# Kernel tuning notes

Hardware: AMD Instinct MI355X
Metric: run time of the kernel (lower is better)

Reference implementation:

```python
import jax, jax.numpy as jnp
import numpy as np

V, E, H = 50000, 300, 128
B, L, QL, NS = 64, 1024, 32, 16
ITERATIONS = 3


def _gru_cell(x, h, w_ih, w_hh, b_ih, b_hh):
    # PyTorch GRUCell math.
    gi = x @ w_ih.T + b_ih
    gh = h @ w_hh.T + b_hh
    i_r, i_z, i_n = jnp.split(gi, 3, axis=-1)
    h_r, h_z, h_n = jnp.split(gh, 3, axis=-1)
    r = jax.nn.sigmoid(i_r + h_r)
    z = jax.nn.sigmoid(i_z + h_z)
    n = jnp.tanh(i_n + r * h_n)
    return (1.0 - z) * n + z * h


def _gru_scan(x, w_ih, w_hh, b_ih, b_hh):
    # x: [B, T, E] -> all hidden states [B, T, H] (nn.GRU, batch_first, h0=0).
    gi = jnp.einsum('bte,ge->btg', x, w_ih) + b_ih  # precompute input gates
    hdim = w_hh.shape[1]

    def step(h, gi_t):
        gh = h @ w_hh.T + b_hh
        i_r, i_z, i_n = jnp.split(gi_t, 3, axis=-1)
        h_r, h_z, h_n = jnp.split(gh, 3, axis=-1)
        r = jax.nn.sigmoid(i_r + h_r)
        z = jax.nn.sigmoid(i_z + h_z)
        n = jnp.tanh(i_n + r * h_n)
        h = (1.0 - z) * n + z * h
        return h, h

    h0 = jnp.zeros((x.shape[0], hdim), x.dtype)
    _, hs = jax.lax.scan(step, h0, jnp.swapaxes(gi, 0, 1))
    return jnp.swapaxes(hs, 0, 1)


def setup_inputs() -> dict:
    key = jax.random.key(0)
    ks = jax.random.split(key, 16)
    x_stories = jax.random.randint(ks[0], (B, L), 1, V)
    # Exactly NS sentence-end marks per story (evenly spaced) -> equal sent counts.
    pos = jnp.arange(1, NS + 1) * (L // NS) - 1
    x_story_masks = jnp.zeros((B, L), bool).at[:, pos].set(True)
    x_questions = jax.random.randint(ks[1], (B, QL), 1, V)
    emb = jax.random.normal(ks[2], (V, E), jnp.float32) * 0.1
    s = float(1.0 / np.sqrt(H))
    u = lambda k, sh: jax.random.uniform(k, sh, jnp.float32, -s, s)
    return {
        'x_stories': x_stories,
        'x_story_masks': x_story_masks,
        'x_questions': x_questions,
        'n_sents': NS,
        'emb': emb,
        'enc_w_ih': u(ks[3], (3 * H, E)),
        'enc_w_hh': u(ks[4], (3 * H, H)),
        'enc_b_ih': u(ks[5], (3 * H,)),
        'enc_b_hh': u(ks[6], (3 * H,)),
        'gate_w': u(ks[7], (1, 4 * H)),
        'gate_b': u(ks[8], (1,)),
        'ep_w_ih': u(ks[9], (3 * H, H)),
        'ep_w_hh': u(ks[10], (3 * H, H)),
        'ep_b_ih': u(ks[11], (3 * H,)),
        'ep_b_hh': u(ks[12], (3 * H,)),
    }


def reference(x_stories, x_story_masks, x_questions, n_sents, emb,
              enc_w_ih, enc_w_hh, enc_b_ih, enc_b_hh,
              gate_w, gate_b, ep_w_ih, ep_w_hh, ep_b_ih, ep_b_hh):
    Bb, Ll = x_stories.shape
    enc_stories = _gru_scan(emb[x_stories], enc_w_ih, enc_w_hh, enc_b_ih, enc_b_hh)  # [B,L,H]
    # Gather the n_sents masked (sentence-end) hidden states per story, in order.
    ar = jnp.arange(Ll)
    sort_key = jnp.where(x_story_masks, ar, Ll + ar)
    idx = jnp.argsort(sort_key, axis=1)[:, :n_sents]  # [B,NS]
    sents = jnp.take_along_axis(enc_stories, idx[:, :, None], axis=1)  # [B,NS,H]
    # Question encoding; pick hidden at the last token before padding.
    q_enc = _gru_scan(emb[x_questions], enc_w_ih, enc_w_hh, enc_b_ih, enc_b_hh)
    next_zero = jnp.concatenate([x_questions[:, 1:] == 0, jnp.ones((Bb, 1), bool)], axis=1)
    qi = jnp.argmax(next_zero, axis=1)
    q_vecs = q_enc[jnp.arange(Bb), qi]  # [B,H]
    q = q_vecs[:, None, :]
    pw1 = sents * q
    d1 = (sents - q) ** 2
    mem = q
    hdim = ep_w_hh.shape[1]
    for _ in range(ITERATIONS):
        pw2 = sents * mem
        d2 = (sents - mem) ** 2
        feats = jnp.concatenate([pw1, pw2, d1, d2], axis=2)  # [B,NS,4H]
        gates = jax.nn.sigmoid(feats @ gate_w.T + gate_b)[..., 0]  # [B,NS]

        def ep_step(h, inp):
            x_t, w_t = inp
            h_new = _gru_cell(x_t, h, ep_w_ih, ep_w_hh, ep_b_ih, ep_b_hh)
            w = w_t[:, None]
            return w * h_new + (1.0 - w) * h, None

        h0 = jnp.zeros((Bb, hdim), sents.dtype)
        ep_state, _ = jax.lax.scan(ep_step, h0, (jnp.swapaxes(sents, 0, 1), gates.T))
        mem = ep_state[:, None, :]
    return q_vecs, ep_state[None], gates
```

## Files before the change

### kernel.cpp

```cpp
#include <hip/hip_runtime.h>
#include <hip/hip_bf16.h>

#define HDIM 128
#define G3 384
#define EDIM 300
#define KP 320
#define ASTRIDE 328
#define BATCH 64
#define LSTO 1024
#define QLEN 32
#define NSENT 16
#define WGB 16
#define HROW 272
#define HBUF (WGB * HROW)

typedef float4 f4;
typedef __attribute__((ext_vector_type(8))) short bf16x8;
typedef __attribute__((ext_vector_type(4))) float f32x4;

__device__ __forceinline__ float sigmf(float x) { return 1.0f / (1.0f + __expf(-x)); }
__device__ __forceinline__ float tanhfast(float x) {
    float e = __expf(-2.0f * x);
    return (1.0f - e) / (1.0f + e);
}
__device__ __forceinline__ float bf2f(unsigned short u) {
    return __uint_as_float(((unsigned)u) << 16);
}
__device__ __forceinline__ unsigned short f2bf_u(float f) {
    union { __hip_bfloat16 b; unsigned short s; } u;
    u.b = __float2bfloat16(f);
    return u.s;
}
__device__ __forceinline__ short f2bf_s(float f) {
    union { __hip_bfloat16 b; short s; } u;
    u.b = __float2bfloat16(f);
    return u.s;
}
__device__ __forceinline__ bf16x8 packrow8(const float* p) {
    bf16x8 v;
#pragma unroll
    for (int i = 0; i < 8; i++) v[i] = f2bf_s(p[i]);
    return v;
}
__device__ __forceinline__ unsigned pack2bf(float a, float b) {
    return ((unsigned)f2bf_u(b) << 16) | (unsigned)f2bf_u(a);
}
__device__ __forceinline__ void barrier_nodrain() {
    asm volatile("" ::: "memory");
    __builtin_amdgcn_s_barrier();
    asm volatile("" ::: "memory");
}
__device__ __forceinline__ void lgkm0() {
    asm volatile("s_waitcnt lgkmcnt(0)" ::: "memory");
    __builtin_amdgcn_sched_barrier(0);
}

__global__ __launch_bounds__(256) void k_w2bf(
    const float* __restrict__ w, __hip_bfloat16* __restrict__ wb, int rows)
{
    int i = blockIdx.x * 256 + threadIdx.x;
    if (i >= rows * KP) return;
    int r = i / KP, k = i - r * KP;
    float v = (k < EDIM) ? w[(size_t)r * EDIM + k] : 0.f;
    wb[i] = __float2bfloat16(v);
}

__global__ __launch_bounds__(512) void k_gi_mfma(
    const int* __restrict__ toks, int nrows,
    const float* __restrict__ emb,
    const __hip_bfloat16* __restrict__ wb, const float* __restrict__ b_ih,
    __hip_bfloat16* __restrict__ gi)
{
    __shared__ __hip_bfloat16 a_lds[32 * ASTRIDE];
    const int tid = threadIdx.x;
    const int rowbase = blockIdx.x * 32;

    for (int i = tid; i < 32 * KP; i += 512) {
        int r = i / KP, k = i - r * KP;
        int row = rowbase + r;
        float v = 0.f;
        if (k < EDIM) {
            int tok = (row < nrows) ? toks[row] : 0;
            v = emb[(size_t)tok * EDIM + k];
        }
        a_lds[r * ASTRIDE + k] = __float2bfloat16(v);
    }
    __syncthreads();

    const int w8   = tid >> 6;
    const int l    = tid & 63;
    const int coln = l & 15;
    const int kg   = l >> 4;

    float bias0 = b_ih[w8 * 48 +  0 + coln];
    float bias1 = b_ih[w8 * 48 + 16 + coln];
    float bias2 = b_ih[w8 * 48 + 32 + coln];

    f32x4 acc[2][3];
#pragma unroll
    for (int mt = 0; mt < 2; mt++) {
        acc[mt][0] = f32x4{bias0, bias0, bias0, bias0};
        acc[mt][1] = f32x4{bias1, bias1, bias1, bias1};
        acc[mt][2] = f32x4{bias2, bias2, bias2, bias2};
    }

    const __hip_bfloat16* bbase = wb + (size_t)(w8 * 48 + coln) * KP + kg * 8;
#pragma unroll
    for (int c = 0; c < KP / 32; ++c) {
        bf16x8 A0 = *reinterpret_cast<const bf16x8*>(
            a_lds + (coln) * ASTRIDE + c * 32 + kg * 8);
        bf16x8 A1 = *reinterpret_cast<const bf16x8*>(
            a_lds + (16 + coln) * ASTRIDE + c * 32 + kg * 8);
        bf16x8 B0 = *reinterpret_cast<const bf16x8*>(bbase + 0 * 16 * KP + c * 32);
        bf16x8 B1 = *reinterpret_cast<const bf16x8*>(bbase + 1 * 16 * KP + c * 32);
        bf16x8 B2 = *reinterpret_cast<const bf16x8*>(bbase + 2 * 16 * KP + c * 32);
        acc[0][0] = __builtin_amdgcn_mfma_f32_16x16x32_bf16(A0, B0, acc[0][0], 0, 0, 0);
        acc[1][0] = __builtin_amdgcn_mfma_f32_16x16x32_bf16(A1, B0, acc[1][0], 0, 0, 0);
        acc[0][1] = __builtin_amdgcn_mfma_f32_16x16x32_bf16(A0, B1, acc[0][1], 0, 0, 0);
        acc[1][1] = __builtin_amdgcn_mfma_f32_16x16x32_bf16(A1, B1, acc[1][1], 0, 0, 0);
        acc[0][2] = __builtin_amdgcn_mfma_f32_16x16x32_bf16(A0, B2, acc[0][2], 0, 0, 0);
        acc[1][2] = __builtin_amdgcn_mfma_f32_16x16x32_bf16(A1, B2, acc[1][2], 0, 0, 0);
    }

#pragma unroll
    for (int mt = 0; mt < 2; mt++) {
#pragma unroll
        for (int nt = 0; nt < 3; nt++) {
            int gate = w8 * 48 + nt * 16 + coln;
#pragma unroll
            for (int q = 0; q < 4; q++) {
                int row = rowbase + mt * 16 + kg * 4 + q;
                if (row < nrows)
                    gi[(size_t)row * G3 + gate] = __float2bfloat16(acc[mt][nt][q]);
            }
        }
    }
}

__global__ __launch_bounds__(192) void k_gi_dense(
    const float* __restrict__ x, int nrows,
    const float* __restrict__ w_ih, const float* __restrict__ b_ih,
    __hip_bfloat16* __restrict__ gi)
{
    __shared__ alignas(16) float a_lds[32 * HDIM];
    int tid = threadIdx.x;
    int rowbase = blockIdx.x * 32;

    for (int i = tid; i < 32 * 32; i += 192) {
        int r = i >> 5, e4 = i & 31;
        int row = rowbase + r;
        f4 v;
        if (row < nrows) v = *reinterpret_cast<const f4*>(x + (size_t)row * HDIM + e4 * 4);
        else { v.x = v.y = v.z = v.w = 0.f; }
        *reinterpret_cast<f4*>(a_lds + r * HDIM + e4 * 4) = v;
    }
    __syncthreads();

    int g0 = tid, g1 = tid + 192;
    const float* w0p = w_ih + (size_t)g0 * HDIM;
    const float* w1p = w_ih + (size_t)g1 * HDIM;
    float bb0 = b_ih[g0], bb1 = b_ih[g1];

#pragma unroll
    for (int half = 0; half < 2; half++) {
        float acc0[16], acc1[16];
#pragma unroll
        for (int r = 0; r < 16; r++) { acc0[r] = 0.f; acc1[r] = 0.f; }

        for (int e4 = 0; e4 < 32; ++e4) {
            f4 w0 = *reinterpret_cast<const f4*>(w0p + e4 * 4);
            f4 w1 = *reinterpret_cast<const f4*>(w1p + e4 * 4);
#pragma unroll
            for (int r = 0; r < 16; r++) {
                f4 a = *reinterpret_cast<const f4*>(
                    a_lds + (half * 16 + r) * HDIM + e4 * 4);
                acc0[r] += a.x * w0.x + a.y * w0.y + a.z * w0.z + a.w * w0.w;
                acc1[r] += a.x * w1.x + a.y * w1.y + a.z * w1.z + a.w * w1.w;
            }
        }
#pragma unroll
        for (int r = 0; r < 16; r++) {
            int row = rowbase + half * 16 + r;
            if (row < nrows) {
                gi[(size_t)row * G3 + g0] = __float2bfloat16(acc0[r] + bb0);
                gi[(size_t)row * G3 + g1] = __float2bfloat16(acc1[r] + bb1);
            }
        }
    }
}

#define SCAN_BODY(TT, TPF, RB, WB, C, P)                                       \
  {                                                                            \
    const int t_ = (TT);                                                       \
    bf16x8 H0 = *reinterpret_cast<const bf16x8*>(h_raw + (RB) + rd0);          \
    bf16x8 H1 = *reinterpret_cast<const bf16x8*>(h_raw + (RB) + rd1);          \
    bf16x8 H2 = *reinterpret_cast<const bf16x8*>(h_raw + (RB) + rd2);          \
    bf16x8 H3 = *reinterpret_cast<const bf16x8*>(h_raw + (RB) + rd3);          \
    {                                                                          \
      const int tp_ = (TPF);                                                   \
      const unsigned short* gp =                                               \
          reinterpret_cast<const unsigned short*>(gib + (size_t)tp_ * G3);     \
      cr##P = *reinterpret_cast<const ushort4*>(gp + j0);                      \
      cz##P = *reinterpret_cast<const ushort4*>(gp + 128 + j0);                \
      cn##P = *reinterpret_cast<const ushort4*>(gp + 256 + j0);                \
      if (MODE == 0) cm##P = mask[bb * LSTO + tp_];                            \
      if (MODE == 2) cw##P = gates[bb * NSENT + tp_];                          \
    }                                                                          \
    f32x4 accr = {br4.x, br4.y, br4.z, br4.w};                                 \
    f32x4 accz = {bz4.x, bz4.y, bz4.z, bz4.w};                                 \
    f32x4 accn = {bn4.x, bn4.y, bn4.z, bn4.w};                                 \
    __builtin_amdgcn_s_setprio(1);                                             \
    accr = __builtin_amdgcn_mfma_f32_16x16x32_bf16(Ar0, H0, accr, 0, 0, 0);    \
    accz = __builtin_amdgcn_mfma_f32_16x16x32_bf16(Az0, H0, accz, 0, 0, 0);    \
    accn = __builtin_amdgcn_mfma_f32_16x16x32_bf16(An0, H0, accn, 0, 0, 0);    \
    accr = __builtin_amdgcn_mfma_f32_16x16x32_bf16(Ar1, H1, accr, 0, 0, 0);    \
    accz = __builtin_amdgcn_mfma_f32_16x16x32_bf16(Az1, H1, accz, 0, 0, 0);    \
    accn = __builtin_amdgcn_mfma_f32_16x16x32_bf16(An1, H1, accn, 0, 0, 0);    \
    accr = __builtin_amdgcn_mfma_f32_16x16x32_bf16(Ar2, H2, accr, 0, 0, 0);    \
    accz = __builtin_amdgcn_mfma_f32_16x16x32_bf16(Az2, H2, accz, 0, 0, 0);    \
    accn = __builtin_amdgcn_mfma_f32_16x16x32_bf16(An2, H2, accn, 0, 0, 0);    \
    accr = __builtin_amdgcn_mfma_f32_16x16x32_bf16(Ar3, H3, accr, 0, 0, 0);    \
    accz = __builtin_amdgcn_mfma_f32_16x16x32_bf16(Az3, H3, accz, 0, 0, 0);    \
    accn = __builtin_amdgcn_mfma_f32_16x16x32_bf16(An3, H3, accn, 0, 0, 0);    \
    __builtin_amdgcn_s_setprio(0);                                             \
    {                                                                          \
      float r0 = sigmf(bf2f(cr##C.x) + accr[0]);                               \
      float r1 = sigmf(bf2f(cr##C.y) + accr[1]);                               \
      float r2 = sigmf(bf2f(cr##C.z) + accr[2]);                               \
      float r3 = sigmf(bf2f(cr##C.w) + accr[3]);                               \
      float z0 = sigmf(bf2f(cz##C.x) + accz[0]);                               \
      float z1 = sigmf(bf2f(cz##C.y) + accz[1]);                               \
      float z2 = sigmf(bf2f(cz##C.z) + accz[2]);                               \
      float z3 = sigmf(bf2f(cz##C.w) + accz[3]);                               \
      float n0 = tanhfast(bf2f(cn##C.x) + r0 * accn[0]);                       \
      float n1 = tanhfast(bf2f(cn##C.y) + r1 * accn[1]);                       \
      float n2 = tanhfast(bf2f(cn##C.z) + r2 * accn[2]);                       \
      float n3 = tanhfast(bf2f(cn##C.w) + r3 * accn[3]);                       \
      float h0 = (1.f - z0) * n0 + z0 * hp0;                                   \
      float h1 = (1.f - z1) * n1 + z1 * hp1;                                   \
      float h2 = (1.f - z2) * n2 + z2 * hp2;                                   \
      float h3 = (1.f - z3) * n3 + z3 * hp3;                                   \
      if (MODE == 2) {                                                         \
        h0 = cw##C * h0 + (1.f - cw##C) * hp0;                                 \
        h1 = cw##C * h1 + (1.f - cw##C) * hp1;                                 \
        h2 = cw##C * h2 + (1.f - cw##C) * hp2;                                 \
        h3 = cw##C * h3 + (1.f - cw##C) * hp3;                                 \
      }                                                                        \
      hp0 = h0; hp1 = h1; hp2 = h2; hp3 = h3;                                  \
    }                                                                          \
    {                                                                          \
      uint2 hw_;                                                               \
      hw_.x = pack2bf(hp0, hp1);                                               \
      hw_.y = pack2bf(hp2, hp3);                                               \
      *reinterpret_cast<uint2*>(h_raw + (WB) + wroff) = hw_;                   \
    }                                                                          \
    if (MODE == 0) {                                                           \
      if (cm##C) {                                                             \
        if (scnt < NSENT) {                                                    \
          float4 v_ = make_float4(hp0, hp1, hp2, hp3);                         \
          *reinterpret_cast<float4*>(                                          \
              sents + ((size_t)bb * NSENT + scnt) * HDIM + j0) = v_;           \
        }                                                                      \
        scnt++;                                                                \
      }                                                                        \
    }                                                                          \
    if (MODE == 1 && t_ == qi) {                                               \
      float4 v_ = make_float4(hp0, hp1, hp2, hp3);                             \
      *reinterpret_cast<float4*>(qv_out + bb * HDIM + j0) = v_;                \
      *reinterpret_cast<float4*>(q_ws + bb * HDIM + j0) = v_;                  \
    }                                                                          \
    if (MODE == 2 && t_ == T - 1) {                                            \
      float4 v_ = make_float4(hp0, hp1, hp2, hp3);                             \
      *reinterpret_cast<float4*>(h_out + bb * HDIM + j0) = v_;                 \
      if (ep_out)                                                              \
        *reinterpret_cast<float4*>(ep_out + bb * HDIM + j0) = v_;              \
    }                                                                          \
    lgkm0();                                                                   \
    barrier_nodrain();                                                         \
  }

template <int MODE>
__global__ __launch_bounds__(512, 2) void k_scan(
    const __hip_bfloat16* __restrict__ gi,
    int T,
    const float* __restrict__ w_hh, const float* __restrict__ b_hh,
    const int* __restrict__ mask,
    float* __restrict__ sents,
    const int* __restrict__ qtoks,
    float* __restrict__ qv_out,
    float* __restrict__ q_ws,
    const float* __restrict__ gates,
    float* __restrict__ h_out,
    float* __restrict__ ep_out)
{
    __shared__ alignas(16) unsigned char h_raw[2 * HBUF];

    const int tid = threadIdx.x;
    const int w   = tid >> 6;
    const int l   = tid & 63;
    const int col = l & 15;
    const int kg  = l >> 4;
    const int b0  = blockIdx.x * WGB;
    const int bb  = b0 + col;
    const int j0  = 16 * w + 4 * kg;

    const float* wr = w_hh + (size_t)(16 * w + col) * HDIM + kg * 8;
    const float* wz = w_hh + (size_t)(128 + 16 * w + col) * HDIM + kg * 8;
    const float* wn = w_hh + (size_t)(256 + 16 * w + col) * HDIM + kg * 8;
    bf16x8 Ar0 = packrow8(wr +  0), Ar1 = packrow8(wr + 32),
           Ar2 = packrow8(wr + 64), Ar3 = packrow8(wr + 96);
    bf16x8 Az0 = packrow8(wz +  0), Az1 = packrow8(wz + 32),
           Az2 = packrow8(wz + 64), Az3 = packrow8(wz + 96);
    bf16x8 An0 = packrow8(wn +  0), An1 = packrow8(wn + 32),
           An2 = packrow8(wn + 64), An3 = packrow8(wn + 96);
    asm volatile("" : "+v"(Ar0), "+v"(Ar1), "+v"(Ar2), "+v"(Ar3));
    asm volatile("" : "+v"(Az0), "+v"(Az1), "+v"(Az2), "+v"(Az3));
    asm volatile("" : "+v"(An0), "+v"(An1), "+v"(An2), "+v"(An3));

    f4 br4 = *reinterpret_cast<const f4*>(b_hh + j0);
    f4 bz4 = *reinterpret_cast<const f4*>(b_hh + 128 + j0);
    f4 bn4 = *reinterpret_cast<const f4*>(b_hh + 256 + j0);

    const int rd0 = col * HROW + 0 * 64 + kg * 16;
    const int rd1 = col * HROW + 1 * 64 + kg * 16;
    const int rd2 = col * HROW + 2 * 64 + kg * 16;
    const int rd3 = col * HROW + 3 * 64 + kg * 16;
    const int wroff = col * HROW + j0 * 2;

    for (int i = tid; i < 2 * HBUF / 4; i += 512)
        reinterpret_cast<unsigned*>(h_raw)[i] = 0u;

    int qi = QLEN - 1;
    if (MODE == 1) {
        for (int t2 = 0; t2 < QLEN - 1; t2++)
            if (qtoks[bb * QLEN + t2 + 1] == 0) { qi = t2; break; }
    }
    int scnt = 0;

    const __hip_bfloat16* gib = gi + (size_t)bb * T * G3;
    ushort4 crA, czA, cnA, crB, czB, cnB;
    int cmA = 0, cmB = 0;
    float cwA = 0.f, cwB = 0.f;
    {
        const unsigned short* gp = reinterpret_cast<const unsigned short*>(gib);
        crA = *reinterpret_cast<const ushort4*>(gp + j0);
        czA = *reinterpret_cast<const ushort4*>(gp + 128 + j0);
        cnA = *reinterpret_cast<const ushort4*>(gp + 256 + j0);
        if (MODE == 0) cmA = mask[bb * LSTO];
        if (MODE == 2) cwA = gates[bb * NSENT];
    }
    float hp0 = 0.f, hp1 = 0.f, hp2 = 0.f, hp3 = 0.f;
    __syncthreads();

    for (int t = 0; t < T; t += 2) {
        SCAN_BODY(t,     t + 1,                     0,    HBUF, A, B)
        SCAN_BODY(t + 1, (t + 2 < T ? t + 2 : t+1), HBUF, 0,    B, A)
    }
}

__global__ __launch_bounds__(128) void k_gates(
    const float* __restrict__ sents, const float* __restrict__ q_ws,
    const float* __restrict__ mem, const float* __restrict__ gate_w,
    const float* __restrict__ gate_b,
    float* __restrict__ gates_ws, float* __restrict__ gout)
{
    int b = blockIdx.x, tid = threadIdx.x;
    int t = tid >> 3, s = tid & 7;
    float p = 0.f;
    const float* sv = sents + ((size_t)b * NSENT + t) * HDIM;
    for (int jj = 0; jj < 16; jj++) {
        int j = s * 16 + jj;
        float S = sv[j], Q = q_ws[b * HDIM + j], M = mem[b * HDIM + j];
        float dq = S - Q, dm = S - M;
        p += (S * Q) * gate_w[j] + (S * M) * gate_w[HDIM + j] +
             (dq * dq) * gate_w[2 * HDIM + j] + (dm * dm) * gate_w[3 * HDIM + j];
    }
    __shared__ float red[16][8];
    red[t][s] = p;
    __syncthreads();
    if (s == 0) {
        float sum = 0.f;
        for (int k = 0; k < 8; k++) sum += red[t][k];
        float gt = sigmf(sum + gate_b[0]);
        gates_ws[b * NSENT + t] = gt;
        if (gout) gout[b * NSENT + t] = gt;
    }
}

extern "C" void kernel_launch(void* const* d_in, const int* in_sizes, int n_in,
                              void* d_out, int out_size, void* d_ws, size_t ws_size,
                              hipStream_t stream)
{
    const int*   x_sto    = (const int*)d_in[0];
    const int*   x_mask   = (const int*)d_in[1];
    const int*   x_q      = (const int*)d_in[2];
    const float* emb      = (const float*)d_in[4];
    const float* enc_w_ih = (const float*)d_in[5];
    const float* enc_w_hh = (const float*)d_in[6];
    const float* enc_b_ih = (const float*)d_in[7];
    const float* enc_b_hh = (const float*)d_in[8];
    const float* gate_w   = (const float*)d_in[9];
    const float* gate_b   = (const float*)d_in[10];
    const float* ep_w_ih  = (const float*)d_in[11];
    const float* ep_w_hh  = (const float*)d_in[12];
    const float* ep_b_ih  = (const float*)d_in[13];
    const float* ep_b_hh  = (const float*)d_in[14];

    float* out_q  = (float*)d_out;
    float* out_ep = (float*)d_out + BATCH * HDIM;
    float* out_g  = (float*)d_out + 2 * BATCH * HDIM;

    char* ws = (char*)d_ws;
    size_t off = 0;
    auto alloc = [&](size_t bytes) {
        void* p = ws + off;
        off += (bytes + 255) & ~(size_t)255;
        return p;
    };
    __hip_bfloat16* gi_sto = (__hip_bfloat16*)alloc((size_t)BATCH * LSTO * G3 * 2);
    __hip_bfloat16* gi_q   = (__hip_bfloat16*)alloc((size_t)BATCH * QLEN * G3 * 2);
    __hip_bfloat16* gi_ep  = (__hip_bfloat16*)alloc((size_t)BATCH * NSENT * G3 * 2);
    __hip_bfloat16* wb_enc = (__hip_bfloat16*)alloc((size_t)G3 * KP * 2);
    float* sents    = (float*)alloc((size_t)BATCH * NSENT * HDIM * 4);
    float* q_ws     = (float*)alloc((size_t)BATCH * HDIM * 4);
    float* mem      = (float*)alloc((size_t)BATCH * HDIM * 4);
    float* gates_ws = (float*)alloc((size_t)BATCH * NSENT * 4);
    (void)ws_size; (void)in_sizes; (void)n_in; (void)out_size;

    k_w2bf<<<(G3 * KP + 255) / 256, 256, 0, stream>>>(enc_w_ih, wb_enc, G3);

    k_gi_mfma<<<(BATCH * LSTO) / 32, 512, 0, stream>>>(
        x_sto, BATCH * LSTO, emb, wb_enc, enc_b_ih, gi_sto);
    k_gi_mfma<<<(BATCH * QLEN) / 32, 512, 0, stream>>>(
        x_q, BATCH * QLEN, emb, wb_enc, enc_b_ih, gi_q);

    k_scan<0><<<BATCH / WGB, 512, 0, stream>>>(
        gi_sto, LSTO, enc_w_hh, enc_b_hh,
        x_mask, sents, nullptr, nullptr, nullptr, nullptr, nullptr, nullptr);
    k_scan<1><<<BATCH / WGB, 512, 0, stream>>>(
        gi_q, QLEN, enc_w_hh, enc_b_hh,
        nullptr, nullptr, x_q, out_q, q_ws, nullptr, nullptr, nullptr);

    k_gi_dense<<<(BATCH * NSENT) / 32, 192, 0, stream>>>(
        sents, BATCH * NSENT, ep_w_ih, ep_b_ih, gi_ep);

    for (int it = 0; it < 3; ++it) {
        const float* msrc = (it == 0) ? q_ws : mem;
        k_gates<<<BATCH, 128, 0, stream>>>(
            sents, q_ws, msrc, gate_w, gate_b, gates_ws,
            (it == 2) ? out_g : nullptr);
        k_scan<2><<<BATCH / WGB, 512, 0, stream>>>(
            gi_ep, NSENT, ep_w_hh, ep_b_hh,
            nullptr, nullptr, nullptr, nullptr, nullptr,
            gates_ws, mem, (it == 2) ? out_ep : nullptr);
    }
}
```

Baseline: 1.375 ms.

## Fuse scans into fewer launches, fold r/z biases into gi, fuse gates with episodic scan

Runs the story and question encoder scans in one 8-block launch, so the short question scan executes alongside the long story scan instead of after it. Folds the hidden r/z biases into the precomputed input gates, so each scan step starts its accumulators from gi and skips one add per element. The gate computation and the episodic GRU scan for all three iterations move into a single kernel that keeps memory and gates in LDS, replacing six small launches. This adds launch_bounds(512,1), extra shared memory and a serial per-thread gate dot product over 128 elements.

```diff
diff --git a/kernel.cpp b/kernel.cpp
--- a/kernel.cpp
+++ b/kernel.cpp
@@ -69,6 +69,7 @@
     const int* __restrict__ toks, int nrows,
     const float* __restrict__ emb,
     const __hip_bfloat16* __restrict__ wb, const float* __restrict__ b_ih,
+    const float* __restrict__ b_hh,
     __hip_bfloat16* __restrict__ gi)
 {
     __shared__ __hip_bfloat16 a_lds[32 * ASTRIDE];
@@ -92,9 +93,10 @@
     const int coln = l & 15;
     const int kg   = l >> 4;
 
-    float bias0 = b_ih[w8 * 48 +  0 + coln];
-    float bias1 = b_ih[w8 * 48 + 16 + coln];
-    float bias2 = b_ih[w8 * 48 + 32 + coln];
+    int g0 = w8 * 48 + coln, g1 = g0 + 16, g2 = g0 + 32;
+    float bias0 = b_ih[g0] + (g0 < 256 ? b_hh[g0] : 0.f);
+    float bias1 = b_ih[g1] + (g1 < 256 ? b_hh[g1] : 0.f);
+    float bias2 = b_ih[g2] + (g2 < 256 ? b_hh[g2] : 0.f);
 
     f32x4 acc[2][3];
 #pragma unroll
@@ -140,6 +142,7 @@
 __global__ __launch_bounds__(192) void k_gi_dense(
     const float* __restrict__ x, int nrows,
     const float* __restrict__ w_ih, const float* __restrict__ b_ih,
+    const float* __restrict__ b_hh,
     __hip_bfloat16* __restrict__ gi)
 {
     __shared__ alignas(16) float a_lds[32 * HDIM];
@@ -159,7 +162,8 @@
     int g0 = tid, g1 = tid + 192;
     const float* w0p = w_ih + (size_t)g0 * HDIM;
     const float* w1p = w_ih + (size_t)g1 * HDIM;
-    float bb0 = b_ih[g0], bb1 = b_ih[g1];
+    float bb0 = b_ih[g0] + (g0 < 256 ? b_hh[g0] : 0.f);
+    float bb1 = b_ih[g1] + (g1 < 256 ? b_hh[g1] : 0.f);
 
 #pragma unroll
     for (int half = 0; half < 2; half++) {
@@ -204,10 +208,10 @@
       cz##P = *reinterpret_cast<const ushort4*>(gp + 128 + j0);                \
       cn##P = *reinterpret_cast<const ushort4*>(gp + 256 + j0);                \
       if (MODE == 0) cm##P = mask[bb * LSTO + tp_];                            \
-      if (MODE == 2) cw##P = gates[bb * NSENT + tp_];                          \
-    }                                                                          \
-    f32x4 accr = {br4.x, br4.y, br4.z, br4.w};                                 \
-    f32x4 accz = {bz4.x, bz4.y, bz4.z, bz4.w};                                 \
+      if (MODE == 2) cw##P = gsrc[tp_];                                        \
+    }                                                                          \
+    f32x4 accr = {bf2f(cr##C.x), bf2f(cr##C.y), bf2f(cr##C.z), bf2f(cr##C.w)};\
+    f32x4 accz = {bf2f(cz##C.x), bf2f(cz##C.y), bf2f(cz##C.z), bf2f(cz##C.w)};\
     f32x4 accn = {bn4.x, bn4.y, bn4.z, bn4.w};                                 \
     __builtin_amdgcn_s_setprio(1);                                             \
     accr = __builtin_amdgcn_mfma_f32_16x16x32_bf16(Ar0, H0, accr, 0, 0, 0);    \
@@ -224,27 +228,27 @@
     accn = __builtin_amdgcn_mfma_f32_16x16x32_bf16(An3, H3, accn, 0, 0, 0);    \
     __builtin_amdgcn_s_setprio(0);                                             \
     {                                                                          \
-      float r0 = sigmf(bf2f(cr##C.x) + accr[0]);                               \
-      float r1 = sigmf(bf2f(cr##C.y) + accr[1]);                               \
-      float r2 = sigmf(bf2f(cr##C.z) + accr[2]);                               \
-      float r3 = sigmf(bf2f(cr##C.w) + accr[3]);                               \
-      float z0 = sigmf(bf2f(cz##C.x) + accz[0]);                               \
-      float z1 = sigmf(bf2f(cz##C.y) + accz[1]);                               \
-      float z2 = sigmf(bf2f(cz##C.z) + accz[2]);                               \
-      float z3 = sigmf(bf2f(cz##C.w) + accz[3]);                               \
+      float r0 = sigmf(accr[0]);                                               \
+      float r1 = sigmf(accr[1]);                                               \
+      float r2 = sigmf(accr[2]);                                               \
+      float r3 = sigmf(accr[3]);                                               \
+      float z0 = sigmf(accz[0]);                                               \
+      float z1 = sigmf(accz[1]);                                               \
+      float z2 = sigmf(accz[2]);                                               \
+      float z3 = sigmf(accz[3]);                                               \
       float n0 = tanhfast(bf2f(cn##C.x) + r0 * accn[0]);                       \
       float n1 = tanhfast(bf2f(cn##C.y) + r1 * accn[1]);                       \
       float n2 = tanhfast(bf2f(cn##C.z) + r2 * accn[2]);                       \
       float n3 = tanhfast(bf2f(cn##C.w) + r3 * accn[3]);                       \
-      float h0 = (1.f - z0) * n0 + z0 * hp0;                                   \
-      float h1 = (1.f - z1) * n1 + z1 * hp1;                                   \
-      float h2 = (1.f - z2) * n2 + z2 * hp2;                                   \
-      float h3 = (1.f - z3) * n3 + z3 * hp3;                                   \
+      float h0 = n0 + z0 * (hp0 - n0);                                         \
+      float h1 = n1 + z1 * (hp1 - n1);                                         \
+      float h2 = n2 + z2 * (hp2 - n2);                                         \
+      float h3 = n3 + z3 * (hp3 - n3);                                         \
       if (MODE == 2) {                                                         \
-        h0 = cw##C * h0 + (1.f - cw##C) * hp0;                                 \
-        h1 = cw##C * h1 + (1.f - cw##C) * hp1;                                 \
-        h2 = cw##C * h2 + (1.f - cw##C) * hp2;                                 \
-        h3 = cw##C * h3 + (1.f - cw##C) * hp3;                                 \
+        h0 = hp0 + cw##C * (h0 - hp0);                                         \
+        h1 = hp1 + cw##C * (h1 - hp1);                                         \
+        h2 = hp2 + cw##C * (h2 - hp2);                                         \
+        h3 = hp3 + cw##C * (h3 - hp3);                                         \
       }                                                                        \
       hp0 = h0; hp1 = h1; hp2 = h2; hp3 = h3;                                  \
     }                                                                          \
@@ -271,7 +275,7 @@
     }                                                                          \
     if (MODE == 2 && t_ == T - 1) {                                            \
       float4 v_ = make_float4(hp0, hp1, hp2, hp3);                             \
-      *reinterpret_cast<float4*>(h_out + bb * HDIM + j0) = v_;                 \
+      *reinterpret_cast<float4*>(mem_lds + col * HDIM + j0) = v_;              \
       if (ep_out)                                                              \
         *reinterpret_cast<float4*>(ep_out + bb * HDIM + j0) = v_;              \
     }                                                                          \
@@ -280,27 +284,22 @@
   }
 
 template <int MODE>
-__global__ __launch_bounds__(512, 2) void k_scan(
-    const __hip_bfloat16* __restrict__ gi,
-    int T,
+__device__ __forceinline__ void scan_core(
+    const __hip_bfloat16* __restrict__ gi, int T,
     const float* __restrict__ w_hh, const float* __restrict__ b_hh,
-    const int* __restrict__ mask,
-    float* __restrict__ sents,
-    const int* __restrict__ qtoks,
-    float* __restrict__ qv_out,
+    const int* __restrict__ mask, float* __restrict__ sents,
+    const int* __restrict__ qtoks, float* __restrict__ qv_out,
     float* __restrict__ q_ws,
-    const float* __restrict__ gates,
-    float* __restrict__ h_out,
-    float* __restrict__ ep_out)
-{
-    __shared__ alignas(16) unsigned char h_raw[2 * HBUF];
-
+    const float* __restrict__ gl_lds,
+    float* __restrict__ ep_out,
+    float* __restrict__ mem_lds,
+    int b0, unsigned char* __restrict__ h_raw)
+{
     const int tid = threadIdx.x;
     const int w   = tid >> 6;
     const int l   = tid & 63;
     const int col = l & 15;
     const int kg  = l >> 4;
-    const int b0  = blockIdx.x * WGB;
     const int bb  = b0 + col;
     const int j0  = 16 * w + 4 * kg;
 
@@ -317,9 +316,8 @@
     asm volatile("" : "+v"(Az0), "+v"(Az1), "+v"(Az2), "+v"(Az3));
     asm volatile("" : "+v"(An0), "+v"(An1), "+v"(An2), "+v"(An3));
 
-    f4 br4 = *reinterpret_cast<const f4*>(b_hh + j0);
-    f4 bz4 = *reinterpret_cast<const f4*>(b_hh + 128 + j0);
     f4 bn4 = *reinterpret_cast<const f4*>(b_hh + 256 + j0);
+    const float* gsrc = (MODE == 2) ? (gl_lds + col * NSENT) : nullptr;
 
     const int rd0 = col * HROW + 0 * 64 + kg * 16;
     const int rd1 = col * HROW + 1 * 64 + kg * 16;
@@ -341,49 +339,84 @@
     ushort4 crA, czA, cnA, crB, czB, cnB;
     int cmA = 0, cmB = 0;
     float cwA = 0.f, cwB = 0.f;
+    __syncthreads();
     {
         const unsigned short* gp = reinterpret_cast<const unsigned short*>(gib);
         crA = *reinterpret_cast<const ushort4*>(gp + j0);
         czA = *reinterpret_cast<const ushort4*>(gp + 128 + j0);
         cnA = *reinterpret_cast<const ushort4*>(gp + 256 + j0);
         if (MODE == 0) cmA = mask[bb * LSTO];
-        if (MODE == 2) cwA = gates[bb * NSENT];
+        if (MODE == 2) cwA = gsrc[0];
     }
     float hp0 = 0.f, hp1 = 0.f, hp2 = 0.f, hp3 = 0.f;
     __syncthreads();
 
     for (int t = 0; t < T; t += 2) {
-        SCAN_BODY(t,     t + 1,                     0,    HBUF, A, B)
-        SCAN_BODY(t + 1, (t + 2 < T ? t + 2 : t+1), HBUF, 0,    B, A)
-    }
-}
-
-__global__ __launch_bounds__(128) void k_gates(
+        SCAN_BODY(t,     t + 1,                       0,    HBUF, A, B)
+        SCAN_BODY(t + 1, (t + 2 < T ? t + 2 : t + 1), HBUF, 0,    B, A)
+    }
+}
+
+__global__ __launch_bounds__(512, 1) void k_scan01(
+    const __hip_bfloat16* __restrict__ gi_sto,
+    const __hip_bfloat16* __restrict__ gi_q,
+    const float* __restrict__ w_hh, const float* __restrict__ b_hh,
+    const int* __restrict__ mask, float* __restrict__ sents,
+    const int* __restrict__ qtoks, float* __restrict__ qv_out,
+    float* __restrict__ q_ws)
+{
+    __shared__ alignas(16) unsigned char h_raw[2 * HBUF];
+    if (blockIdx.x < 4) {
+        scan_core<0>(gi_sto, LSTO, w_hh, b_hh, mask, sents,
+                     nullptr, nullptr, nullptr, nullptr, nullptr, nullptr,
+                     blockIdx.x * WGB, h_raw);
+    } else {
+        scan_core<1>(gi_q, QLEN, w_hh, b_hh, nullptr, nullptr,
+                     qtoks, qv_out, q_ws, nullptr, nullptr, nullptr,
+                     (blockIdx.x - 4) * WGB, h_raw);
+    }
+}
+
+__global__ __launch_bounds__(512, 1) void k_ep(
+    const __hip_bfloat16* __restrict__ gi_ep,
+    const float* __restrict__ w_hh, const float* __restrict__ b_hh,
     const float* __restrict__ sents, const float* __restrict__ q_ws,
-    const float* __restrict__ mem, const float* __restrict__ gate_w,
-    const float* __restrict__ gate_b,
-    float* __restrict__ gates_ws, float* __restrict__ gout)
-{
-    int b = blockIdx.x, tid = threadIdx.x;
-    int t = tid >> 3, s = tid & 7;
-    float p = 0.f;
-    const float* sv = sents + ((size_t)b * NSENT + t) * HDIM;
-    for (int jj = 0; jj < 16; jj++) {
-        int j = s * 16 + jj;
-        float S = sv[j], Q = q_ws[b * HDIM + j], M = mem[b * HDIM + j];
-        float dq = S - Q, dm = S - M;
-        p += (S * Q) * gate_w[j] + (S * M) * gate_w[HDIM + j] +
-             (dq * dq) * gate_w[2 * HDIM + j] + (dm * dm) * gate_w[3 * HDIM + j];
-    }
-    __shared__ float red[16][8];
-    red[t][s] = p;
-    __syncthreads();
-    if (s == 0) {
-        float sum = 0.f;
-        for (int k = 0; k < 8; k++) sum += red[t][k];
-        float gt = sigmf(sum + gate_b[0]);
-        gates_ws[b * NSENT + t] = gt;
-        if (gout) gout[b * NSENT + t] = gt;
+    const float* __restrict__ gate_w, const float* __restrict__ gate_b,
+    float* __restrict__ out_g, float* __restrict__ out_ep)
+{
+    __shared__ alignas(16) unsigned char h_raw[2 * HBUF];
+    __shared__ float gl[WGB * NSENT];
+    __shared__ alignas(16) float mem_lds[WGB * HDIM];
+
+    const int tid = threadIdx.x;
+    const int b0 = blockIdx.x * WGB;
+    const float gb0 = gate_b[0];
+
+    for (int it = 0; it < 3; ++it) {
+        if (tid < 256) {
+            int bq = tid >> 4, tq = tid & 15;
+            int b = b0 + bq;
+            const float* sv = sents + ((size_t)b * NSENT + tq) * HDIM;
+            const float* Qv = q_ws + (size_t)b * HDIM;
+            const float* Mv = mem_lds + bq * HDIM;
+            float p = 0.f;
+            for (int j = 0; j < HDIM; j++) {
+                float S = sv[j], Q = Qv[j];
+                float M = (it == 0) ? Q : Mv[j];
+                float dq = S - Q, dm = S - M;
+                p += (S * Q) * gate_w[j] + (S * M) * gate_w[HDIM + j] +
+                     (dq * dq) * gate_w[2 * HDIM + j] +
+                     (dm * dm) * gate_w[3 * HDIM + j];
+            }
+            float g = sigmf(p + gb0);
+            gl[bq * NSENT + tq] = g;
+            if (it == 2) out_g[b * NSENT + tq] = g;
+        }
+        scan_core<2>(gi_ep, NSENT, w_hh, b_hh, nullptr, nullptr,
+                     nullptr, nullptr, nullptr, gl,
+                     (it == 2) ? out_ep : nullptr, mem_lds,
+                     b0, h_raw);
+        __syncthreads();
     }
 }
 
@@ -423,35 +456,20 @@
     __hip_bfloat16* wb_enc = (__hip_bfloat16*)alloc((size_t)G3 * KP * 2);
     float* sents    = (float*)alloc((size_t)BATCH * NSENT * HDIM * 4);
     float* q_ws     = (float*)alloc((size_t)BATCH * HDIM * 4);
-    float* mem      = (float*)alloc((size_t)BATCH * HDIM * 4);
-    float* gates_ws = (float*)alloc((size_t)BATCH * NSENT * 4);
     (void)ws_size; (void)in_sizes; (void)n_in; (void)out_size;
 
     k_w2bf<<<(G3 * KP + 255) / 256, 256, 0, stream>>>(enc_w_ih, wb_enc, G3);
 
     k_gi_mfma<<<(BATCH * LSTO) / 32, 512, 0, stream>>>(
-        x_sto, BATCH * LSTO, emb, wb_enc, enc_b_ih, gi_sto);
+        x_sto, BATCH * LSTO, emb, wb_enc, enc_b_ih, enc_b_hh, gi_sto);
     k_gi_mfma<<<(BATCH * QLEN) / 32, 512, 0, stream>>>(
-        x_q, BATCH * QLEN, emb, wb_enc, enc_b_ih, gi_q);
-
-    k_scan<0><<<BATCH / WGB, 512, 0, stream>>>(
-        gi_sto, LSTO, enc_w_hh, enc_b_hh,
-        x_mask, sents, nullptr, nullptr, nullptr, nullptr, nullptr, nullptr);
-    k_scan<1><<<BATCH / WGB, 512, 0, stream>>>(
-        gi_q, QLEN, enc_w_hh, enc_b_hh,
-        nullptr, nullptr, x_q, out_q, q_ws, nullptr, nullptr, nullptr);
+        x_q, BATCH * QLEN, emb, wb_enc, enc_b_ih, enc_b_hh, gi_q);
+
+    k_scan01<<<8, 512, 0, stream>>>(
+        gi_sto, gi_q, enc_w_hh, enc_b_hh, x_mask, sents, x_q, out_q, q_ws);
 
     k_gi_dense<<<(BATCH * NSENT) / 32, 192, 0, stream>>>(
-        sents, BATCH * NSENT, ep_w_ih, ep_b_ih, gi_ep);
-
-    for (int it = 0; it < 3; ++it) {
-        const float* msrc = (it == 0) ? q_ws : mem;
-        k_gates<<<BATCH, 128, 0, stream>>>(
-            sents, q_ws, msrc, gate_w, gate_b, gates_ws,
-            (it == 2) ? out_g : nullptr);
-        k_scan<2><<<BATCH / WGB, 512, 0, stream>>>(
-            gi_ep, NSENT, ep_w_hh, ep_b_hh,
-            nullptr, nullptr, nullptr, nullptr, nullptr,
-            gates_ws, mem, (it == 2) ? out_ep : nullptr);
-    }
-}
+        sents, BATCH * NSENT, ep_w_ih, ep_b_ih, ep_b_hh, gi_ep);
+    k_ep<<<BATCH / WGB, 512, 0, stream>>>(
+        gi_ep, ep_w_hh, ep_b_hh, sents, q_ws, gate_w, gate_b, out_g, out_ep);
+}
```

New measurement: 1.307 ms. 1.05x faster.
